# Optimization experiments

Measured on AMD Instinct MI355X. Metric: run time of the kernel, lower is better.

The kernel has to match this reference:

```python
import jax, jax.numpy as jnp
import numpy as np

N = 4096      # num_nodes
U = 64        # num_units
IN = 2        # input_dim
DIM = U + IN  # 66
H = 4         # attention heads
ALPHA = 0.2   # leaky slope inside attention scores
SLOPE = 0.01  # nn.LeakyReLU() default for subnet activations
NEG_INF = -9e15


def setup_inputs() -> dict:
    key = jax.random.key(0)
    ks = jax.random.split(key, 20)
    def gn(k, shape, fan):
        return jax.random.normal(k, shape, dtype=jnp.float32) / np.float32(np.sqrt(fan))
    adj = jax.random.randint(ks[2], (N, N), 0, 2, dtype=jnp.int32)
    adj = jnp.maximum(adj, jnp.eye(N, dtype=jnp.int32))  # ensure self-loops
    return {
        "inputs": jax.random.normal(ks[0], (1, N * IN), dtype=jnp.float32),
        "hx": jax.random.normal(ks[1], (1, N, U), dtype=jnp.float32),
        "adj": adj,
        "m1_W": gn(ks[3], (H, DIM, DIM), DIM),
        "m1_a1": gn(ks[4], (H, DIM), DIM),
        "m1_a2": gn(ks[5], (H, DIM), DIM),
        "m1_Wout": gn(ks[6], (H * DIM, DIM), H * DIM),
        "m1_ao1": gn(ks[7], (DIM,), DIM),
        "m1_ao2": gn(ks[8], (DIM,), DIM),
        "m2_W": gn(ks[9], (H, DIM, DIM), DIM),
        "m2_a1": gn(ks[10], (H, DIM), DIM),
        "m2_a2": gn(ks[11], (H, DIM), DIM),
        "m2_Wout": gn(ks[12], (H * DIM, DIM), H * DIM),
        "m2_ao1": gn(ks[13], (DIM,), DIM),
        "m2_ao2": gn(ks[14], (DIM,), DIM),
        "g1_W": gn(ks[15], (DIM, 2 * U), DIM),
        "g1_b": jnp.zeros((2 * U,), dtype=jnp.float32),
        "g2_W": gn(ks[16], (DIM, U), DIM),
        "g2_b": jnp.zeros((U,), dtype=jnp.float32),
    }


def gat_layer(x, W, a1, a2, mask):
    # x: [N,Fin], W: [Fin,Fout], a1/a2: [Fout], mask: [N,N] bool
    h = x @ W                                   # [N,Fout]
    f1 = h @ a1                                 # [N] source term
    f2 = h @ a2                                 # [N] target term
    e = jax.nn.leaky_relu(f1[:, None] + f2[None, :], ALPHA)  # [N,N]
    e = jnp.where(mask, e, NEG_INF)
    attn = jax.nn.softmax(e, axis=-1)
    return attn @ h                             # [N,Fout]


def subnet(x, W, a1, a2, Wout, ao1, ao2, mask):
    # multi-head GAT, concat heads, activation, output GAT layer, activation
    heads = jax.vmap(gat_layer, in_axes=(None, 0, 0, 0, None))(x, W, a1, a2, mask)  # [H,N,DIM]
    hcat = jnp.transpose(heads, (1, 0, 2)).reshape(x.shape[0], -1)                   # [N,H*DIM]
    hcat = jax.nn.leaky_relu(hcat, SLOPE)
    out = gat_layer(hcat, Wout, ao1, ao2, mask)                                      # [N,DIM]
    return jax.nn.leaky_relu(out, SLOPE)


def reference(inputs, hx, adj, m1_W, m1_a1, m1_a2, m1_Wout, m1_ao1, m1_ao2,
              m2_W, m2_a1, m2_a2, m2_Wout, m2_ao1, m2_ao2,
              g1_W, g1_b, g2_W, g2_b):
    mask = adj > 0
    xi = inputs.reshape(N, IN)
    xh = hx.reshape(N, U)
    # _GAT1: concat(inputs, hx) -> GATSubNet1 -> linear -> sigmoid -> split r,u
    x1 = jnp.concatenate([xi, xh], axis=-1)                 # [N,DIM]
    g1 = subnet(x1, m1_W, m1_a1, m1_a2, m1_Wout, m1_ao1, m1_ao2, mask)
    value = jax.nn.sigmoid(g1 @ g1_W + g1_b)                # [N,2U]
    r, u = value[:, :U], value[:, U:]
    # _GAT2: concat(inputs, r*hx) -> GATSubNet2 -> linear -> tanh
    x2 = jnp.concatenate([xi, r * xh], axis=-1)             # [N,DIM]
    g2 = subnet(x2, m2_W, m2_a1, m2_a2, m2_Wout, m2_ao1, m2_ao2, mask)
    c = jnp.tanh(g2 @ g2_W + g2_b)                          # [N,U]
    new_state = u * xh + (1.0 - u) * c
    return new_state.reshape(1, N, U)
```

## Files before the change

### kernel.cpp

```cpp
#include <hip/hip_runtime.h>
#include <hip/hip_bf16.h>

constexpr int kN = 4096;
constexpr int kDim = 66;
constexpr int kH = 4;
constexpr int kU = 64;
constexpr float kAlpha = 0.2f;
constexpr float kSlope = 0.01f;

typedef __attribute__((ext_vector_type(8))) short short8;
typedef __attribute__((ext_vector_type(4))) float floatx4;

__device__ inline unsigned short f2bf(float x){
  unsigned int u = __float_as_uint(x);
  unsigned int r = (u + 0x7FFFu + ((u >> 16) & 1u)) >> 16;
  return (unsigned short)r;
}

__global__ void pack_adj_k(const int* __restrict__ adj, unsigned long long* __restrict__ packed){
  int gid = blockIdx.x * 256 + threadIdx.x;
  unsigned long long m = __ballot(adj[gid] != 0);
  if ((threadIdx.x & 63) == 0) packed[gid >> 6] = m;
}

__global__ void prep_x_k(const float* __restrict__ in2, const float* __restrict__ hx,
                         unsigned short* __restrict__ x1b, unsigned short* __restrict__ x2b){
  int i = blockIdx.x * 4 + (threadIdx.x >> 6);
  int c = threadIdx.x & 63;
  x1b[(size_t)i * 96 + 2 + c] = f2bf(hx[(size_t)i * kU + c]);
  if (c < 2){
    unsigned short xv = f2bf(in2[i * 2 + c]);
    x1b[(size_t)i * 96 + c] = xv;
    x2b[(size_t)i * 96 + c] = xv;
  }
}

__global__ void bbuild_k(const float* __restrict__ m1W, const float* __restrict__ m1a1, const float* __restrict__ m1a2,
                         const float* __restrict__ m1Wo, const float* __restrict__ m1ao1, const float* __restrict__ m1ao2,
                         const float* __restrict__ m2W, const float* __restrict__ m2a1, const float* __restrict__ m2a2,
                         const float* __restrict__ m2Wo, const float* __restrict__ m2ao1, const float* __restrict__ m2ao2,
                         const float* __restrict__ g1W, const float* __restrict__ g1b,
                         const float* __restrict__ g2W, const float* __restrict__ g2b,
                         unsigned short* __restrict__ B1t, unsigned short* __restrict__ B1t2,
                         unsigned short* __restrict__ B2t, unsigned short* __restrict__ B2t2,
                         unsigned short* __restrict__ Bgt, unsigned short* __restrict__ Bft){
  int b = blockIdx.x, t = threadIdx.x;
  if (b < 8){
    int m = b & 3;
    const float* W  = (b < 4 ? m1W  : m2W)  + (size_t)m * kDim * kDim;
    const float* a1 = (b < 4 ? m1a1 : m2a1) + m * kDim;
    const float* a2 = (b < 4 ? m1a2 : m2a2) + m * kDim;
    unsigned short* Bo = (b < 4 ? B1t : B1t2) + (size_t)m * 80 * 96;
    __shared__ float Ws[kDim * kDim];
    __shared__ float wa1s[kDim], wa2s[kDim];
    for (int z = t; z < kDim * kDim; z += 256) Ws[z] = W[z];
    __syncthreads();
    if (t < kDim){
      float s1 = 0.f, s2 = 0.f;
      for (int d = 0; d < kDim; d++){ float wv = Ws[t * kDim + d]; s1 += wv * a1[d]; s2 += wv * a2[d]; }
      wa1s[t] = s1; wa2s[t] = s2;
    }
    __syncthreads();
    for (int z = t; z < 80 * 96; z += 256){
      int nn = z / 96, k = z % 96;
      float val = 0.f;
      if (k < kDim){
        if (nn < kDim) val = Ws[k * kDim + nn];
        else if (nn == 66) val = wa1s[k];
        else if (nn == 67) val = wa2s[k];
      }
      Bo[z] = f2bf(val);
    }
  } else if (b < 10){
    const float* Wo  = (b == 8 ? m1Wo  : m2Wo);
    const float* ao1 = (b == 8 ? m1ao1 : m2ao1);
    const float* ao2 = (b == 8 ? m1ao2 : m2ao2);
    unsigned short* Bo = (b == 8 ? B2t : B2t2);
    __shared__ float wo1s[264], wo2s[264];
    for (int k = t; k < 264; k += 256){
      float s1 = 0.f, s2 = 0.f;
      for (int d = 0; d < kDim; d++){ float wv = Wo[(size_t)k * kDim + d]; s1 += wv * ao1[d]; s2 += wv * ao2[d]; }
      wo1s[k] = s1; wo2s[k] = s2;
    }
    __syncthreads();
    for (int z = t; z < 80 * 288; z += 256){
      int nn = z / 288, k = z % 288;
      float val = 0.f;
      if (k < 264){
        if (nn < kDim) val = Wo[(size_t)k * kDim + nn];
        else if (nn == 66) val = wo1s[k];
        else if (nn == 67) val = wo2s[k];
      }
      Bo[z] = f2bf(val);
    }
  } else if (b == 10){
    for (int z = t; z < 128 * 96; z += 256){
      int nn = z / 96, k = z % 96;
      float val = 0.f;
      if (k < kDim) val = g1W[k * 128 + nn];
      else if (k == 66) val = g1b[nn];
      Bgt[z] = f2bf(val);
    }
  } else {
    for (int z = t; z < 64 * 96; z += 256){
      int nn = z / 96, k = z % 96;
      float val = 0.f;
      if (k < kDim) val = g2W[k * 64 + nn];
      else if (k == 66) val = g2b[nn];
      Bft[z] = f2bf(val);
    }
  }
}

template<int KSTEPS, int NT, int EPI>
__global__ __launch_bounds__(256) void gemm_k(
    const unsigned short* __restrict__ A, const unsigned short* __restrict__ Bt,
    void* __restrict__ p0, void* __restrict__ p1, void* __restrict__ p2,
    const float* __restrict__ aux)
{
  constexpr int KP = KSTEPS * 32;
  const int m = blockIdx.y;
  const int i0 = blockIdx.x * 64;
  const int t = threadIdx.x;
  const int w = t >> 6, lane = t & 63, q = lane >> 4, n = lane & 15;
  const int arow = i0 + w * 16 + n;
  const unsigned short* Ar = A + (size_t)arow * KP;
  const unsigned short* Bm = Bt + (size_t)m * (NT * 16) * KP;
  floatx4 acc[NT];
  #pragma unroll
  for (int v = 0; v < NT; v++) acc[v] = (floatx4){0.f, 0.f, 0.f, 0.f};
  #pragma unroll
  for (int ks = 0; ks < KSTEPS; ks++){
    short8 af = *(const short8*)&Ar[ks * 32 + q * 8];
    #pragma unroll
    for (int nt = 0; nt < NT; nt++){
      short8 bf = *(const short8*)&Bm[(size_t)(nt * 16 + n) * KP + ks * 32 + q * 8];
      acc[nt] = __builtin_amdgcn_mfma_f32_16x16x32_bf16(af, bf, acc[nt], 0, 0, 0);
    }
  }
  const int ib = i0 + w * 16 + q * 4;
  if constexpr (EPI == 0){
    unsigned short* Ht = (unsigned short*)p0 + (size_t)m * 80 * kN;
    float* f1 = (float*)p1 + (size_t)m * kN;
    float* f2 = (float*)p2 + (size_t)m * kN;
    #pragma unroll
    for (int nt = 0; nt < NT; nt++){
      int c = nt * 16 + n;
      if (c < kDim){
        uint2 pk;
        pk.x = ((unsigned)f2bf(acc[nt][1]) << 16) | f2bf(acc[nt][0]);
        pk.y = ((unsigned)f2bf(acc[nt][3]) << 16) | f2bf(acc[nt][2]);
        *(uint2*)&Ht[(size_t)c * kN + ib] = pk;
      } else if (c == 66){
        float4 fv; fv.x = acc[nt][0]; fv.y = acc[nt][1]; fv.z = acc[nt][2]; fv.w = acc[nt][3];
        *(float4*)&f1[ib] = fv;
        *(uint2*)&Ht[(size_t)66 * kN + ib] = make_uint2(0x3F803F80u, 0x3F803F80u);
      } else if (c == 67){
        float4 fv; fv.x = acc[nt][0]; fv.y = acc[nt][1]; fv.z = acc[nt][2]; fv.w = acc[nt][3];
        *(float4*)&f2[ib] = fv;
        *(uint2*)&Ht[(size_t)67 * kN + ib] = make_uint2(0u, 0u);
      } else {
        *(uint2*)&Ht[(size_t)c * kN + ib] = make_uint2(0u, 0u);
      }
    }
  } else if constexpr (EPI == 1){
    float* u = (float*)p0;
    unsigned short* x2b = (unsigned short*)p1;
    #pragma unroll
    for (int nt = 0; nt < NT; nt++){
      int c = nt * 16 + n;
      #pragma unroll
      for (int r = 0; r < 4; r++){
        float v = 1.f / (1.f + __expf(-acc[nt][r]));
        if (c < 64) x2b[(size_t)(ib + r) * 96 + 2 + c] = f2bf(v * aux[(size_t)(ib + r) * kU + c]);
        else        u[(size_t)(ib + r) * kU + (c - 64)] = v;
      }
    }
  } else {
    float* outp = (float*)p0;
    const float* u = (const float*)p1;
    #pragma unroll
    for (int nt = 0; nt < NT; nt++){
      int c = nt * 16 + n;
      #pragma unroll
      for (int r = 0; r < 4; r++){
        float cc = tanhf(acc[nt][r]);
        float uv = u[(size_t)(ib + r) * kU + c];
        outp[(size_t)(ib + r) * kU + c] = uv * aux[(size_t)(ib + r) * kU + c] + (1.f - uv) * cc;
      }
    }
  }
}

__global__ void reduce_max_k(const float* __restrict__ f2, float* __restrict__ fmax){
  int m = blockIdx.x;
  const float* p = f2 + (size_t)m * kN;
  float v = -1e30f;
  for (int j = threadIdx.x; j < kN; j += 256) v = fmaxf(v, p[j]);
  #pragma unroll
  for (int o = 32; o; o >>= 1) v = fmaxf(v, __shfl_down(v, o));
  __shared__ float s[4];
  if ((threadIdx.x & 63) == 0) s[threadIdx.x >> 6] = v;
  __syncthreads();
  if (threadIdx.x == 0) fmax[m] = fmaxf(fmaxf(s[0], s[1]), fmaxf(s[2], s[3]));
}

__global__ __launch_bounds__(256, 4) void attn_mfma_k(
    const unsigned short* __restrict__ Ht, const float* __restrict__ f1,
    const float* __restrict__ f2, const float* __restrict__ fmax,
    const unsigned long long* __restrict__ packed,
    float* __restrict__ pacc)
{
  const int m = blockIdx.y, js = blockIdx.z;
  const int i0 = blockIdx.x * 64;
  const int t = threadIdx.x;
  const int w = t >> 6, lane = t & 63, q = lane >> 4, n = lane & 15;
  const int i = i0 + w * 16 + n;
  const unsigned short* Hg = Ht + (size_t)m * 80 * kN;
  const float* f2m = f2 + (size_t)m * kN;
  const float f1v = f1[(size_t)m * kN + i];
  const float t0 = f1v + fmax[m];
  const float S = fmaxf(t0, kAlpha * t0);

  __shared__ __align__(16) unsigned short HtL[80 * 136];
  __shared__ __align__(16) float f2s[128];

  floatx4 acc[5];
  #pragma unroll
  for (int v = 0; v < 5; v++) acc[v] = (floatx4){0.f, 0.f, 0.f, 0.f};

  const int jbase = js * 1024;
  const unsigned long long* prow = packed + (size_t)i * 64;
  for (int ch = 0; ch < 8; ch++){
    const int j0 = jbase + ch * 128;
    __syncthreads();
    for (int z = t; z < 80 * 16; z += 256){
      int row = z >> 4, c16 = z & 15;
      *(uint4*)&HtL[row * 136 + c16 * 8] = *(const uint4*)&Hg[(size_t)row * kN + j0 + c16 * 8];
    }
    if (t < 128) f2s[t] = f2m[j0 + t];
    __syncthreads();
    unsigned long long w0 = prow[(j0 >> 6)];
    unsigned long long w1 = prow[(j0 >> 6) + 1];
    #pragma unroll
    for (int ks = 0; ks < 4; ks++){
      unsigned long long wsel = (ks < 2) ? w0 : w1;
      unsigned int bits = (unsigned int)((wsel >> ((ks & 1) * 32 + q * 8)) & 0xffull);
      float4 fa = *(const float4*)&f2s[ks * 32 + q * 8];
      float4 fb = *(const float4*)&f2s[ks * 32 + q * 8 + 4];
      float fv[8] = {fa.x, fa.y, fa.z, fa.w, fb.x, fb.y, fb.z, fb.w};
      float p[8];
      #pragma unroll
      for (int e = 0; e < 8; e++){
        float tt = f1v + fv[e];
        float ee = fmaxf(tt, kAlpha * tt);
        float pv = __expf(ee - S);
        p[e] = ((bits >> e) & 1u) ? pv : 0.f;
      }
      union { short8 s; unsigned int u[4]; } af;
      #pragma unroll
      for (int e2 = 0; e2 < 4; e2++)
        af.u[e2] = __builtin_amdgcn_perm(__float_as_uint(p[2 * e2 + 1]), __float_as_uint(p[2 * e2]), 0x07060302u);
      #pragma unroll
      for (int nt = 0; nt < 5; nt++){
        const short8 bf = *(const short8*)&HtL[(nt * 16 + n) * 136 + ks * 32 + q * 8];
        acc[nt] = __builtin_amdgcn_mfma_f32_16x16x32_bf16(af.s, bf, acc[nt], 0, 0, 0);
      }
    }
  }
  float* pw = pacc + ((size_t)(m * 4 + js) * kN + (i0 + w * 16)) * 80;
  #pragma unroll
  for (int nt = 0; nt < 5; nt++){
    #pragma unroll
    for (int r = 0; r < 4; r++)
      pw[(q * 4 + r) * 80 + nt * 16 + n] = acc[nt][r];
  }
}

__global__ void combine_k(const float* __restrict__ pacc, unsigned short* __restrict__ outb,
                          int ostride, int ones_col){
  int m = blockIdx.y;
  int i = blockIdx.x * 64 + (threadIdx.x >> 2);
  int cg = threadIdx.x & 3;
  const float* p0 = pacc + ((size_t)(m * 4) * kN + i) * 80;
  const float* p1 = p0 + (size_t)kN * 80;
  const float* p2 = p1 + (size_t)kN * 80;
  const float* p3 = p2 + (size_t)kN * 80;
  float l = p0[66] + p1[66] + p2[66] + p3[66];
  float inv = 1.f / l;
  unsigned short* orow = outb + (size_t)i * ostride + m * kDim;
  #pragma unroll
  for (int cc = 0; cc < 17; cc++){
    int c = cg * 17 + cc;
    if (c < kDim){
      float v = (p0[c] + p1[c] + p2[c] + p3[c]) * inv;
      v = fmaxf(v, kSlope * v);
      orow[c] = f2bf(v);
    }
  }
  if (ones_col && cg == 3) orow[66] = 0x3F80;
}

extern "C" void kernel_launch(void* const* d_in, const int* in_sizes, int n_in,
                              void* d_out, int out_size, void* d_ws, size_t ws_size,
                              hipStream_t stream){
  const float* inputs  = (const float*)d_in[0];
  const float* hx      = (const float*)d_in[1];
  const int*   adj     = (const int*)d_in[2];
  const float* m1_W    = (const float*)d_in[3];
  const float* m1_a1   = (const float*)d_in[4];
  const float* m1_a2   = (const float*)d_in[5];
  const float* m1_Wout = (const float*)d_in[6];
  const float* m1_ao1  = (const float*)d_in[7];
  const float* m1_ao2  = (const float*)d_in[8];
  const float* m2_W    = (const float*)d_in[9];
  const float* m2_a1   = (const float*)d_in[10];
  const float* m2_a2   = (const float*)d_in[11];
  const float* m2_Wout = (const float*)d_in[12];
  const float* m2_ao1  = (const float*)d_in[13];
  const float* m2_ao2  = (const float*)d_in[14];
  const float* g1_W    = (const float*)d_in[15];
  const float* g1_b    = (const float*)d_in[16];
  const float* g2_W    = (const float*)d_in[17];
  const float* g2_b    = (const float*)d_in[18];
  float* out = (float*)d_out;

  char* ws = (char*)d_ws;
  size_t off = 0;
  auto alloc = [&](size_t bytes) -> void* {
    void* p = ws + off;
    off = (off + bytes + 255) & ~(size_t)255;
    return p;
  };
  unsigned long long* packed = (unsigned long long*)alloc((size_t)kN * 64 * 8);
  unsigned short* x1b  = (unsigned short*)alloc((size_t)kN * 96 * 2);
  unsigned short* x2b  = (unsigned short*)alloc((size_t)kN * 96 * 2);
  unsigned short* Ht   = (unsigned short*)alloc((size_t)kH * 80 * kN * 2);
  unsigned short* Hto  = (unsigned short*)alloc((size_t)80 * kN * 2);
  unsigned short* hcatb= (unsigned short*)alloc((size_t)kN * 288 * 2);
  unsigned short* gb   = (unsigned short*)alloc((size_t)kN * 96 * 2);
  unsigned short* g2b  = (unsigned short*)alloc((size_t)kN * 96 * 2);
  float* f1   = (float*)alloc((size_t)kH * kN * 4);
  float* f2   = (float*)alloc((size_t)kH * kN * 4);
  float* fo1  = (float*)alloc((size_t)kN * 4);
  float* fo2  = (float*)alloc((size_t)kN * 4);
  float* fmax = (float*)alloc(64);
  float* u    = (float*)alloc((size_t)kN * kU * 4);
  float* pacc = (float*)alloc((size_t)16 * kN * 80 * 4);
  unsigned short* B1t  = (unsigned short*)alloc((size_t)kH * 80 * 96 * 2);
  unsigned short* B1t2 = (unsigned short*)alloc((size_t)kH * 80 * 96 * 2);
  unsigned short* B2t  = (unsigned short*)alloc((size_t)80 * 288 * 2);
  unsigned short* B2t2 = (unsigned short*)alloc((size_t)80 * 288 * 2);
  unsigned short* Bgt  = (unsigned short*)alloc((size_t)128 * 96 * 2);
  unsigned short* Bft  = (unsigned short*)alloc((size_t)64 * 96 * 2);
  (void)ws_size; (void)in_sizes; (void)n_in; (void)out_size;

  pack_adj_k<<<kN * kN / 256, 256, 0, stream>>>(adj, packed);
  prep_x_k<<<kN / 4, 256, 0, stream>>>(inputs, hx, x1b, x2b);
  bbuild_k<<<12, 256, 0, stream>>>(m1_W, m1_a1, m1_a2, m1_Wout, m1_ao1, m1_ao2,
                                   m2_W, m2_a1, m2_a2, m2_Wout, m2_ao1, m2_ao2,
                                   g1_W, g1_b, g2_W, g2_b,
                                   B1t, B1t2, B2t, B2t2, Bgt, Bft);

  gemm_k<3, 5, 0><<<dim3(64, kH), 256, 0, stream>>>(x1b, B1t, Ht, f1, f2, nullptr);
  reduce_max_k<<<kH, 256, 0, stream>>>(f2, fmax);
  attn_mfma_k<<<dim3(64, kH, 4), 256, 0, stream>>>(Ht, f1, f2, fmax, packed, pacc);
  combine_k<<<dim3(64, kH), 256, 0, stream>>>(pacc, hcatb, 288, 0);
  gemm_k<9, 5, 0><<<dim3(64, 1), 256, 0, stream>>>(hcatb, B2t, Hto, fo1, fo2, nullptr);
  reduce_max_k<<<1, 256, 0, stream>>>(fo2, fmax + 4);
  attn_mfma_k<<<dim3(64, 1, 4), 256, 0, stream>>>(Hto, fo1, fo2, fmax + 4, packed, pacc);
  combine_k<<<dim3(64, 1), 256, 0, stream>>>(pacc, gb, 96, 1);
  gemm_k<3, 8, 1><<<dim3(64, 1), 256, 0, stream>>>(gb, Bgt, u, x2b, nullptr, hx);

  gemm_k<3, 5, 0><<<dim3(64, kH), 256, 0, stream>>>(x2b, B1t2, Ht, f1, f2, nullptr);
  reduce_max_k<<<kH, 256, 0, stream>>>(f2, fmax);
  attn_mfma_k<<<dim3(64, kH, 4), 256, 0, stream>>>(Ht, f1, f2, fmax, packed, pacc);
  combine_k<<<dim3(64, kH), 256, 0, stream>>>(pacc, hcatb, 288, 0);
  gemm_k<9, 5, 0><<<dim3(64, 1), 256, 0, stream>>>(hcatb, B2t2, Hto, fo1, fo2, nullptr);
  reduce_max_k<<<1, 256, 0, stream>>>(fo2, fmax + 4);
  attn_mfma_k<<<dim3(64, 1, 4), 256, 0, stream>>>(Hto, fo1, fo2, fmax + 4, packed, pacc);
  combine_k<<<dim3(64, 1), 256, 0, stream>>>(pacc, g2b, 96, 1);
  gemm_k<3, 4, 2><<<dim3(64, 1), 256, 0, stream>>>(g2b, Bft, out, u, nullptr, hx);
}
```

Baseline: 363.1 us.

## Fuse setup kernels, fold max reduction into GEMM, store partials in bf16

Merges the adjacency-packing, input-prep and weight-building kernels into one launch. The separate reduce_max kernels are removed: each GEMM epilogue now does an atomicMax on order-preserving integer keys, using a buffer that the setup kernel zeroes. Attention scores are pre-scaled by log2(e) so the inner loop can use the hardware exp2. Split-K attention partials are stored as bf16 instead of fp32, which halves partial traffic but costs some precision in the accumulated sums and the denominator.

```diff
diff --git a/kernel.cpp b/kernel.cpp
--- a/kernel.cpp
+++ b/kernel.cpp
@@ -7,6 +7,7 @@
 constexpr int kU = 64;
 constexpr float kAlpha = 0.2f;
 constexpr float kSlope = 0.01f;
+constexpr float kLog2e = 1.44269504f;
 
 typedef __attribute__((ext_vector_type(8))) short short8;
 typedef __attribute__((ext_vector_type(4))) float floatx4;
@@ -16,35 +17,50 @@
   unsigned int r = (u + 0x7FFFu + ((u >> 16) & 1u)) >> 16;
   return (unsigned short)r;
 }
-
-__global__ void pack_adj_k(const int* __restrict__ adj, unsigned long long* __restrict__ packed){
-  int gid = blockIdx.x * 256 + threadIdx.x;
-  unsigned long long m = __ballot(adj[gid] != 0);
-  if ((threadIdx.x & 63) == 0) packed[gid >> 6] = m;
-}
-
-__global__ void prep_x_k(const float* __restrict__ in2, const float* __restrict__ hx,
-                         unsigned short* __restrict__ x1b, unsigned short* __restrict__ x2b){
-  int i = blockIdx.x * 4 + (threadIdx.x >> 6);
-  int c = threadIdx.x & 63;
-  x1b[(size_t)i * 96 + 2 + c] = f2bf(hx[(size_t)i * kU + c]);
-  if (c < 2){
-    unsigned short xv = f2bf(in2[i * 2 + c]);
-    x1b[(size_t)i * 96 + c] = xv;
-    x2b[(size_t)i * 96 + c] = xv;
-  }
-}
-
-__global__ void bbuild_k(const float* __restrict__ m1W, const float* __restrict__ m1a1, const float* __restrict__ m1a2,
-                         const float* __restrict__ m1Wo, const float* __restrict__ m1ao1, const float* __restrict__ m1ao2,
-                         const float* __restrict__ m2W, const float* __restrict__ m2a1, const float* __restrict__ m2a2,
-                         const float* __restrict__ m2Wo, const float* __restrict__ m2ao1, const float* __restrict__ m2ao2,
-                         const float* __restrict__ g1W, const float* __restrict__ g1b,
-                         const float* __restrict__ g2W, const float* __restrict__ g2b,
-                         unsigned short* __restrict__ B1t, unsigned short* __restrict__ B1t2,
-                         unsigned short* __restrict__ B2t, unsigned short* __restrict__ B2t2,
-                         unsigned short* __restrict__ Bgt, unsigned short* __restrict__ Bft){
-  int b = blockIdx.x, t = threadIdx.x;
+__device__ inline float bf2f(unsigned short v){
+  return __uint_as_float((unsigned int)v << 16);
+}
+__device__ inline unsigned int fkey(float f){
+  unsigned int u = __float_as_uint(f);
+  return (u & 0x80000000u) ? ~u : (u | 0x80000000u);
+}
+__device__ inline float funkey(unsigned int k){
+  unsigned int u = (k & 0x80000000u) ? (k ^ 0x80000000u) : ~k;
+  return __uint_as_float(u);
+}
+
+__global__ void setup_k(const int* __restrict__ adj, unsigned long long* __restrict__ packed,
+                        const float* __restrict__ in2, const float* __restrict__ hx,
+                        unsigned short* __restrict__ x1b, unsigned short* __restrict__ x2b,
+                        const float* __restrict__ m1W, const float* __restrict__ m1a1, const float* __restrict__ m1a2,
+                        const float* __restrict__ m1Wo, const float* __restrict__ m1ao1, const float* __restrict__ m1ao2,
+                        const float* __restrict__ m2W, const float* __restrict__ m2a1, const float* __restrict__ m2a2,
+                        const float* __restrict__ m2Wo, const float* __restrict__ m2ao1, const float* __restrict__ m2ao2,
+                        const float* __restrict__ g1W, const float* __restrict__ g1b,
+                        const float* __restrict__ g2W, const float* __restrict__ g2b,
+                        unsigned short* __restrict__ B1t, unsigned short* __restrict__ B1t2,
+                        unsigned short* __restrict__ B2t, unsigned short* __restrict__ B2t2,
+                        unsigned short* __restrict__ Bgt, unsigned short* __restrict__ Bft,
+                        unsigned int* __restrict__ fmaxbuf){
+  int bb = blockIdx.x, t = threadIdx.x;
+  if (bb < 16384){
+    int gid = bb * 256 + t;
+    unsigned long long m = __ballot(adj[gid] != 0);
+    if ((t & 63) == 0) packed[gid >> 6] = m;
+    return;
+  }
+  if (bb < 16384 + 1024){
+    int i = (bb - 16384) * 4 + (t >> 6);
+    int c = t & 63;
+    x1b[(size_t)i * 96 + 2 + c] = f2bf(hx[(size_t)i * kU + c]);
+    if (c < 2){
+      unsigned short xv = f2bf(in2[i * 2 + c]);
+      x1b[(size_t)i * 96 + c] = xv;
+      x2b[(size_t)i * 96 + c] = xv;
+    }
+    return;
+  }
+  int b = bb - (16384 + 1024);
   if (b < 8){
     int m = b & 3;
     const float* W  = (b < 4 ? m1W  : m2W)  + (size_t)m * kDim * kDim;
@@ -102,6 +118,7 @@
       Bgt[z] = f2bf(val);
     }
   } else {
+    if (t < 16) fmaxbuf[t] = 0u;
     for (int z = t; z < 64 * 96; z += 256){
       int nn = z / 96, k = z % 96;
       float val = 0.f;
@@ -116,7 +133,7 @@
 __global__ __launch_bounds__(256) void gemm_k(
     const unsigned short* __restrict__ A, const unsigned short* __restrict__ Bt,
     void* __restrict__ p0, void* __restrict__ p1, void* __restrict__ p2,
-    const float* __restrict__ aux)
+    const float* __restrict__ aux, unsigned int* __restrict__ fmaxp)
 {
   constexpr int KP = KSTEPS * 32;
   const int m = blockIdx.y;
@@ -143,6 +160,7 @@
     unsigned short* Ht = (unsigned short*)p0 + (size_t)m * 80 * kN;
     float* f1 = (float*)p1 + (size_t)m * kN;
     float* f2 = (float*)p2 + (size_t)m * kN;
+    float lm = -3e38f;
     #pragma unroll
     for (int nt = 0; nt < NT; nt++){
       int c = nt * 16 + n;
@@ -152,17 +170,23 @@
         pk.y = ((unsigned)f2bf(acc[nt][3]) << 16) | f2bf(acc[nt][2]);
         *(uint2*)&Ht[(size_t)c * kN + ib] = pk;
       } else if (c == 66){
-        float4 fv; fv.x = acc[nt][0]; fv.y = acc[nt][1]; fv.z = acc[nt][2]; fv.w = acc[nt][3];
+        float4 fv; fv.x = acc[nt][0] * kLog2e; fv.y = acc[nt][1] * kLog2e;
+        fv.z = acc[nt][2] * kLog2e; fv.w = acc[nt][3] * kLog2e;
         *(float4*)&f1[ib] = fv;
         *(uint2*)&Ht[(size_t)66 * kN + ib] = make_uint2(0x3F803F80u, 0x3F803F80u);
       } else if (c == 67){
-        float4 fv; fv.x = acc[nt][0]; fv.y = acc[nt][1]; fv.z = acc[nt][2]; fv.w = acc[nt][3];
+        float4 fv; fv.x = acc[nt][0] * kLog2e; fv.y = acc[nt][1] * kLog2e;
+        fv.z = acc[nt][2] * kLog2e; fv.w = acc[nt][3] * kLog2e;
         *(float4*)&f2[ib] = fv;
+        lm = fmaxf(fmaxf(fv.x, fv.y), fmaxf(fv.z, fv.w));
         *(uint2*)&Ht[(size_t)67 * kN + ib] = make_uint2(0u, 0u);
       } else {
         *(uint2*)&Ht[(size_t)c * kN + ib] = make_uint2(0u, 0u);
       }
     }
+    lm = fmaxf(lm, __shfl_xor(lm, 16));
+    lm = fmaxf(lm, __shfl_xor(lm, 32));
+    if (lane == 3) atomicMax(&fmaxp[m], fkey(lm));
   } else if constexpr (EPI == 1){
     float* u = (float*)p0;
     unsigned short* x2b = (unsigned short*)p1;
@@ -192,24 +216,11 @@
   }
 }
 
-__global__ void reduce_max_k(const float* __restrict__ f2, float* __restrict__ fmax){
-  int m = blockIdx.x;
-  const float* p = f2 + (size_t)m * kN;
-  float v = -1e30f;
-  for (int j = threadIdx.x; j < kN; j += 256) v = fmaxf(v, p[j]);
-  #pragma unroll
-  for (int o = 32; o; o >>= 1) v = fmaxf(v, __shfl_down(v, o));
-  __shared__ float s[4];
-  if ((threadIdx.x & 63) == 0) s[threadIdx.x >> 6] = v;
-  __syncthreads();
-  if (threadIdx.x == 0) fmax[m] = fmaxf(fmaxf(s[0], s[1]), fmaxf(s[2], s[3]));
-}
-
 __global__ __launch_bounds__(256, 4) void attn_mfma_k(
     const unsigned short* __restrict__ Ht, const float* __restrict__ f1,
-    const float* __restrict__ f2, const float* __restrict__ fmax,
+    const float* __restrict__ f2, const unsigned int* __restrict__ fmaxu,
     const unsigned long long* __restrict__ packed,
-    float* __restrict__ pacc)
+    unsigned short* __restrict__ paccb)
 {
   const int m = blockIdx.y, js = blockIdx.z;
   const int i0 = blockIdx.x * 64;
@@ -219,7 +230,8 @@
   const unsigned short* Hg = Ht + (size_t)m * 80 * kN;
   const float* f2m = f2 + (size_t)m * kN;
   const float f1v = f1[(size_t)m * kN + i];
-  const float t0 = f1v + fmax[m];
+  const float fmx = funkey(fmaxu[m]);
+  const float t0 = f1v + fmx;
   const float S = fmaxf(t0, kAlpha * t0);
 
   __shared__ __align__(16) unsigned short HtL[80 * 136];
@@ -254,7 +266,7 @@
       for (int e = 0; e < 8; e++){
         float tt = f1v + fv[e];
         float ee = fmaxf(tt, kAlpha * tt);
-        float pv = __expf(ee - S);
+        float pv = __builtin_amdgcn_exp2f(ee - S);
         p[e] = ((bits >> e) & 1u) ? pv : 0.f;
       }
       union { short8 s; unsigned int u[4]; } af;
@@ -268,32 +280,32 @@
       }
     }
   }
-  float* pw = pacc + ((size_t)(m * 4 + js) * kN + (i0 + w * 16)) * 80;
+  unsigned short* pw = paccb + ((size_t)(m * 4 + js) * kN + (i0 + w * 16)) * 80;
   #pragma unroll
   for (int nt = 0; nt < 5; nt++){
     #pragma unroll
     for (int r = 0; r < 4; r++)
-      pw[(q * 4 + r) * 80 + nt * 16 + n] = acc[nt][r];
-  }
-}
-
-__global__ void combine_k(const float* __restrict__ pacc, unsigned short* __restrict__ outb,
+      pw[(q * 4 + r) * 80 + nt * 16 + n] = f2bf(acc[nt][r]);
+  }
+}
+
+__global__ void combine_k(const unsigned short* __restrict__ paccb, unsigned short* __restrict__ outb,
                           int ostride, int ones_col){
   int m = blockIdx.y;
   int i = blockIdx.x * 64 + (threadIdx.x >> 2);
   int cg = threadIdx.x & 3;
-  const float* p0 = pacc + ((size_t)(m * 4) * kN + i) * 80;
-  const float* p1 = p0 + (size_t)kN * 80;
-  const float* p2 = p1 + (size_t)kN * 80;
-  const float* p3 = p2 + (size_t)kN * 80;
-  float l = p0[66] + p1[66] + p2[66] + p3[66];
+  const unsigned short* p0 = paccb + ((size_t)(m * 4) * kN + i) * 80;
+  const unsigned short* p1 = p0 + (size_t)kN * 80;
+  const unsigned short* p2 = p1 + (size_t)kN * 80;
+  const unsigned short* p3 = p2 + (size_t)kN * 80;
+  float l = bf2f(p0[66]) + bf2f(p1[66]) + bf2f(p2[66]) + bf2f(p3[66]);
   float inv = 1.f / l;
   unsigned short* orow = outb + (size_t)i * ostride + m * kDim;
   #pragma unroll
   for (int cc = 0; cc < 17; cc++){
     int c = cg * 17 + cc;
     if (c < kDim){
-      float v = (p0[c] + p1[c] + p2[c] + p3[c]) * inv;
+      float v = (bf2f(p0[c]) + bf2f(p1[c]) + bf2f(p2[c]) + bf2f(p3[c])) * inv;
       v = fmaxf(v, kSlope * v);
       orow[c] = f2bf(v);
     }
@@ -344,9 +356,9 @@
   float* f2   = (float*)alloc((size_t)kH * kN * 4);
   float* fo1  = (float*)alloc((size_t)kN * 4);
   float* fo2  = (float*)alloc((size_t)kN * 4);
-  float* fmax = (float*)alloc(64);
+  unsigned int* fmaxbuf = (unsigned int*)alloc(64);
   float* u    = (float*)alloc((size_t)kN * kU * 4);
-  float* pacc = (float*)alloc((size_t)16 * kN * 80 * 4);
+  unsigned short* paccb = (unsigned short*)alloc((size_t)16 * kN * 80 * 2);
   unsigned short* B1t  = (unsigned short*)alloc((size_t)kH * 80 * 96 * 2);
   unsigned short* B1t2 = (unsigned short*)alloc((size_t)kH * 80 * 96 * 2);
   unsigned short* B2t  = (unsigned short*)alloc((size_t)80 * 288 * 2);
@@ -355,30 +367,25 @@
   unsigned short* Bft  = (unsigned short*)alloc((size_t)64 * 96 * 2);
   (void)ws_size; (void)in_sizes; (void)n_in; (void)out_size;
 
-  pack_adj_k<<<kN * kN / 256, 256, 0, stream>>>(adj, packed);
-  prep_x_k<<<kN / 4, 256, 0, stream>>>(inputs, hx, x1b, x2b);
-  bbuild_k<<<12, 256, 0, stream>>>(m1_W, m1_a1, m1_a2, m1_Wout, m1_ao1, m1_ao2,
-                                   m2_W, m2_a1, m2_a2, m2_Wout, m2_ao1, m2_ao2,
-                                   g1_W, g1_b, g2_W, g2_b,
-                                   B1t, B1t2, B2t, B2t2, Bgt, Bft);
-
-  gemm_k<3, 5, 0><<<dim3(64, kH), 256, 0, stream>>>(x1b, B1t, Ht, f1, f2, nullptr);
-  reduce_max_k<<<kH, 256, 0, stream>>>(f2, fmax);
-  attn_mfma_k<<<dim3(64, kH, 4), 256, 0, stream>>>(Ht, f1, f2, fmax, packed, pacc);
-  combine_k<<<dim3(64, kH), 256, 0, stream>>>(pacc, hcatb, 288, 0);
-  gemm_k<9, 5, 0><<<dim3(64, 1), 256, 0, stream>>>(hcatb, B2t, Hto, fo1, fo2, nullptr);
-  reduce_max_k<<<1, 256, 0, stream>>>(fo2, fmax + 4);
-  attn_mfma_k<<<dim3(64, 1, 4), 256, 0, stream>>>(Hto, fo1, fo2, fmax + 4, packed, pacc);
-  combine_k<<<dim3(64, 1), 256, 0, stream>>>(pacc, gb, 96, 1);
-  gemm_k<3, 8, 1><<<dim3(64, 1), 256, 0, stream>>>(gb, Bgt, u, x2b, nullptr, hx);
-
-  gemm_k<3, 5, 0><<<dim3(64, kH), 256, 0, stream>>>(x2b, B1t2, Ht, f1, f2, nullptr);
-  reduce_max_k<<<kH, 256, 0, stream>>>(f2, fmax);
-  attn_mfma_k<<<dim3(64, kH, 4), 256, 0, stream>>>(Ht, f1, f2, fmax, packed, pacc);
-  combine_k<<<dim3(64, kH), 256, 0, stream>>>(pacc, hcatb, 288, 0);
-  gemm_k<9, 5, 0><<<dim3(64, 1), 256, 0, stream>>>(hcatb, B2t2, Hto, fo1, fo2, nullptr);
-  reduce_max_k<<<1, 256, 0, stream>>>(fo2, fmax + 4);
-  attn_mfma_k<<<dim3(64, 1, 4), 256, 0, stream>>>(Hto, fo1, fo2, fmax + 4, packed, pacc);
-  combine_k<<<dim3(64, 1), 256, 0, stream>>>(pacc, g2b, 96, 1);
-  gemm_k<3, 4, 2><<<dim3(64, 1), 256, 0, stream>>>(g2b, Bft, out, u, nullptr, hx);
-}
+  setup_k<<<16384 + 1024 + 12, 256, 0, stream>>>(adj, packed, inputs, hx, x1b, x2b,
+      m1_W, m1_a1, m1_a2, m1_Wout, m1_ao1, m1_ao2,
+      m2_W, m2_a1, m2_a2, m2_Wout, m2_ao1, m2_ao2,
+      g1_W, g1_b, g2_W, g2_b,
+      B1t, B1t2, B2t, B2t2, Bgt, Bft, fmaxbuf);
+
+  gemm_k<3, 5, 0><<<dim3(64, kH), 256, 0, stream>>>(x1b, B1t, Ht, f1, f2, nullptr, fmaxbuf + 0);
+  attn_mfma_k<<<dim3(64, kH, 4), 256, 0, stream>>>(Ht, f1, f2, fmaxbuf + 0, packed, paccb);
+  combine_k<<<dim3(64, kH), 256, 0, stream>>>(paccb, hcatb, 288, 0);
+  gemm_k<9, 5, 0><<<dim3(64, 1), 256, 0, stream>>>(hcatb, B2t, Hto, fo1, fo2, nullptr, fmaxbuf + 4);
+  attn_mfma_k<<<dim3(64, 1, 4), 256, 0, stream>>>(Hto, fo1, fo2, fmaxbuf + 4, packed, paccb);
+  combine_k<<<dim3(64, 1), 256, 0, stream>>>(paccb, gb, 96, 1);
+  gemm_k<3, 8, 1><<<dim3(64, 1), 256, 0, stream>>>(gb, Bgt, u, x2b, nullptr, hx, nullptr);
+
+  gemm_k<3, 5, 0><<<dim3(64, kH), 256, 0, stream>>>(x2b, B1t2, Ht, f1, f2, nullptr, fmaxbuf + 5);
+  attn_mfma_k<<<dim3(64, kH, 4), 256, 0, stream>>>(Ht, f1, f2, fmaxbuf + 5, packed, paccb);
+  combine_k<<<dim3(64, kH), 256, 0, stream>>>(paccb, hcatb, 288, 0);
+  gemm_k<9, 5, 0><<<dim3(64, 1), 256, 0, stream>>>(hcatb, B2t2, Hto, fo1, fo2, nullptr, fmaxbuf + 9);
+  attn_mfma_k<<<dim3(64, 1, 4), 256, 0, stream>>>(Hto, fo1, fo2, fmaxbuf + 9, packed, paccb);
+  combine_k<<<dim3(64, 1), 256, 0, stream>>>(paccb, g2b, 96, 1);
+  gemm_k<3, 4, 2><<<dim3(64, 1), 256, 0, stream>>>(g2b, Bft, out, u, nullptr, hx, nullptr);
+}
```

New measurement: 349.3 us. -3.8%, faster.
